# Optimization experiments

Hardware: AMD Instinct MI355X
Metric: run time of the kernel (lower is better)

Reference implementation:

```python
import jax, jax.numpy as jnp
import numpy as np


def blockdiag_matmul(x, w):
    """Block-diagonal (Monarch) linear: w has shape (nblocks, out_blk, in_blk);
    x has shape (..., nblocks*in_blk); returns (..., nblocks*out_blk)."""
    nb, q, p = w.shape
    lead = x.shape[:-1]
    xb = x.reshape(-1, nb, p)  # (tokens, nblocks, in_blk)
    out = jnp.einsum('bnp,nqp->bnq', xb, w)  # per-block matmul
    return out.reshape(*lead, nb * q)


def setup_inputs() -> dict:
    key = jax.random.key(0)
    k_x, k1, k2, k3 = jax.random.split(key, 4)
    B, S, D = 4, 4096, 2048
    NB, FF = 4, 8192  # nblocks, adjusted intermediate size
    # Kaiming-uniform-like scale for block weights (fan_in = D or FF per block-row)
    s1 = 1.0 / np.sqrt(D)
    s2 = 1.0 / np.sqrt(FF)
    return {
        'x': jax.random.normal(k_x, (B, S, D), dtype=jnp.float32),
        'w1': jax.random.normal(k1, (NB, FF // NB, D // NB), dtype=jnp.float32) * s1,
        'w3': jax.random.normal(k3, (NB, FF // NB, D // NB), dtype=jnp.float32) * s1,
        'w2': jax.random.normal(k2, (NB, D // NB, FF // NB), dtype=jnp.float32) * s2,
    }


def reference(x, w1, w3, w2):
    # SwiGLU MLP: w2(silu(w1(x)) * w3(x)), all projections block-diagonal
    gate = jax.nn.silu(blockdiag_matmul(x, w1))
    up = blockdiag_matmul(x, w3)
    return blockdiag_matmul(gate * up, w2)
```

## Files before the change

### kernel.cpp

```cpp
#include <hip/hip_runtime.h>
#include <cstdint>

typedef __attribute__((ext_vector_type(8))) short bf16x8;
typedef __attribute__((ext_vector_type(4))) float f32x4;
typedef unsigned short u16;

#define RD(p) (*(const bf16x8*)(p))

__device__ inline u16 f2bf(float f) {
  union { float f; unsigned int u; } v; v.f = f;
  unsigned int u = v.u;
  unsigned int r = (u + 0x7fffu + ((u >> 16) & 1u)) >> 16;
  return (u16)r;
}

__device__ inline void gload_lds16(const u16* g, u16* l) {
  __builtin_amdgcn_global_load_lds(
      (const __attribute__((address_space(1))) void*)g,
      (__attribute__((address_space(3))) void*)l, 16, 0, 0);
}

#define PH_BEGIN() \
  __builtin_amdgcn_s_barrier(); \
  asm volatile("s_waitcnt lgkmcnt(0)" ::: "memory"); \
  __builtin_amdgcn_s_setprio(1)
#define PH_END() \
  __builtin_amdgcn_s_setprio(0); \
  __builtin_amdgcn_s_barrier()

__global__ void cvt_f32_bf16(const float* __restrict__ src, u16* __restrict__ dst, int n8) {
  int i = blockIdx.x * blockDim.x + threadIdx.x;
  int stride = gridDim.x * blockDim.x;
  for (; i < n8; i += stride) {
    const float4* s = (const float4*)(src + (size_t)i * 8);
    float4 a = s[0], b = s[1];
    union { u16 h[8]; uint4 v; } o;
    o.h[0] = f2bf(a.x); o.h[1] = f2bf(a.y); o.h[2] = f2bf(a.z); o.h[3] = f2bf(a.w);
    o.h[4] = f2bf(b.x); o.h[5] = f2bf(b.y); o.h[6] = f2bf(b.z); o.h[7] = f2bf(b.w);
    *(uint4*)(dst + (size_t)i * 8) = o.v;
  }
}

__global__ void cvt_w3x(const float* __restrict__ s0, const float* __restrict__ s1,
                        const float* __restrict__ s2, u16* __restrict__ d0,
                        u16* __restrict__ d1, u16* __restrict__ d2) {
  const int n8 = 524288;
  int i = blockIdx.x * blockDim.x + threadIdx.x;
  int stride = gridDim.x * blockDim.x;
  for (; i < 3 * n8; i += stride) {
    int seg = i / n8;
    int j = i - seg * n8;
    const float* src = (seg == 0) ? s0 : (seg == 1) ? s1 : s2;
    u16* dst = (seg == 0) ? d0 : (seg == 1) ? d1 : d2;
    const float4* s = (const float4*)(src + (size_t)j * 8);
    float4 a = s[0], b = s[1];
    union { u16 h[8]; uint4 v; } o;
    o.h[0] = f2bf(a.x); o.h[1] = f2bf(a.y); o.h[2] = f2bf(a.z); o.h[3] = f2bf(a.w);
    o.h[4] = f2bf(b.x); o.h[5] = f2bf(b.y); o.h[6] = f2bf(b.z); o.h[7] = f2bf(b.w);
    *(uint4*)(dst + (size_t)j * 8) = o.v;
  }
}

__launch_bounds__(512, 2)
__global__ void gemm_gateup8(const u16* __restrict__ xb, const u16* __restrict__ w1b,
                             const u16* __restrict__ w3b, u16* __restrict__ hout) {
  constexpr int NT = 8;
  constexpr int TPB = 4;
  constexpr int TOT = NT * TPB;
  __shared__ __attribute__((aligned(16))) u16 lA[2][256 * 64];
  __shared__ __attribute__((aligned(16))) u16 lB[2][2][128 * 64];

  int bid = blockIdx.x;
  int sw = (bid & 7) * 128 + (bid >> 3);
  int nblk = sw >> 8;
  int rem = sw & 255;
  int mt = rem >> 2, ntg = rem & 3;

  int tid = threadIdx.x, w = tid >> 6, ln = tid & 63;
  int wr = w >> 1, wc = w & 1;
  int l15 = ln & 15, l4 = ln >> 4;
  int lr = ln >> 3, ln8 = ln & 7;

  int cx0 = ((l4 ^ (l15 & 7)) << 4);
  int cx1 = (((4 + l4) ^ (l15 & 7)) << 4);
  int aOff0 = (wr * 64 + l15) * 128 + cx0;
  int aOff1 = (wr * 64 + l15) * 128 + cx1;
  int bOff0 = (wc * 64 + l15) * 128 + cx0;
  int bOff1 = (wc * 64 + l15) * 128 + cx1;

  int u0t = w * 8, u1t = 64 + w * 8;
  int rbA0 = ((u0t >> 5) << 6) + (u0t & 31);
  int rbA1 = ((u1t >> 5) << 6) + (u1t & 31);
  int dA0 = rbA0 * 128, dA1 = rbA1 * 128;
  int dB0 = u0t * 128, dB1 = u1t * 128;
  int gaA0 = rbA0 * 2048, gaA1 = rbA1 * 2048;
  int gaB0 = u0t * 512, gaB1 = u1t * 512;
  int swzg = (ln8 ^ lr) << 3;

  const u16* gA  = xb  + (size_t)(mt * 256) * 2048 + nblk * 512 + lr * 2048 + swzg;
  const u16* gB1 = w1b + (size_t)nblk * (2048 * 512) + (size_t)(ntg * 512) * 512 + lr * 512 + swzg;
  const u16* gB3 = w3b + (size_t)nblk * (2048 * 512) + (size_t)(ntg * 512) * 512 + lr * 512 + swzg;

  #define OFFA(s) (((s) & 7) * 64)
  #define OFFB(s) ((((s) >> 3) << 16) + (((s) & 7) * 64))

  f32x4 acc1[4][4], acc3[4][4];
#pragma unroll
  for (int i = 0; i < 4; i++)
#pragma unroll
    for (int j = 0; j < 4; j++) {
      acc1[i][j] = (f32x4){0.f, 0.f, 0.f, 0.f};
      acc3[i][j] = (f32x4){0.f, 0.f, 0.f, 0.f};
    }

  gload_lds16(gA + gaA0,              (u16*)((char*)lA + dA0));
  gload_lds16(gA + gaA1,              (u16*)((char*)lA + dA1));
  gload_lds16(gB3 + gaB0,             (u16*)((char*)lB + 16384 + dB0));
  gload_lds16(gB3 + gaB1,             (u16*)((char*)lB + 16384 + dB1));
  gload_lds16(gA + gaA0 + 65536,      (u16*)((char*)lA + dA0 + 4096));
  gload_lds16(gA + gaA1 + 65536,      (u16*)((char*)lA + dA1 + 4096));
  gload_lds16(gB1 + gaB0,             (u16*)((char*)lB + dB0));
  gload_lds16(gB1 + gaB1,             (u16*)((char*)lB + dB1));
  gload_lds16(gA + OFFA(1) + gaA0,          (u16*)((char*)lA + 32768 + dA0));
  gload_lds16(gA + OFFA(1) + gaA1,          (u16*)((char*)lA + 32768 + dA1));
  gload_lds16(gB3 + OFFB(1) + gaB0,         (u16*)((char*)lB + 32768 + 16384 + dB0));
  gload_lds16(gB3 + OFFB(1) + gaB1,         (u16*)((char*)lB + 32768 + 16384 + dB1));
  gload_lds16(gA + OFFA(1) + gaA0 + 65536,  (u16*)((char*)lA + 32768 + dA0 + 4096));
  gload_lds16(gA + OFFA(1) + gaA1 + 65536,  (u16*)((char*)lA + 32768 + dA1 + 4096));
  asm volatile("s_waitcnt vmcnt(6)" ::: "memory");
  __builtin_amdgcn_s_barrier();

  int sCur = 0, sNxt = 32768;
  bf16x8 aT[2][2], aH[2][2], b1[4][2], b3[4][2];

  for (int kt = 0; kt < TOT; ++kt) {
    const char* pA0 = (const char*)lA + (sCur + aOff0);
    const char* pA1 = (const char*)lA + (sCur + aOff1);
    const char* pB0 = (const char*)lB + (sCur + bOff0);
    const char* pB1p = (const char*)lB + (sCur + bOff1);
    int s1 = kt + 1, s2 = kt + 2;
    int oA2 = OFFA(s2), oB1n = OFFB(s1), oB32 = OFFB(s2);
    bool q1 = (s1 < TOT), q2 = (s2 < TOT);

#pragma unroll
    for (int f = 0; f < 2; ++f) {
      aT[f][0] = RD(pA0 + f * 2048); aT[f][1] = RD(pA1 + f * 2048);
    }
#pragma unroll
    for (int g = 0; g < 4; ++g) {
      b1[g][0] = RD(pB0 + g * 2048); b1[g][1] = RD(pB1p + g * 2048);
    }
    if (q1) {
      gload_lds16(gB1 + oB1n + gaB0, (u16*)((char*)lB + sNxt + dB0));
      gload_lds16(gB1 + oB1n + gaB1, (u16*)((char*)lB + sNxt + dB1));
    }
    asm volatile("s_waitcnt lgkmcnt(8)" ::: "memory");
    PH_BEGIN();
#pragma unroll
    for (int f = 0; f < 2; ++f)
#pragma unroll
      for (int g = 0; g < 4; ++g)
#pragma unroll
        for (int ks = 0; ks < 2; ++ks)
          acc1[f][g] = __builtin_amdgcn_mfma_f32_16x16x32_bf16(b1[g][ks], aT[f][ks], acc1[f][g], 0, 0, 0);
    PH_END();

#pragma unroll
    for (int g = 0; g < 4; ++g) {
      b3[g][0] = RD(pB0 + 16384 + g * 2048); b3[g][1] = RD(pB1p + 16384 + g * 2048);
    }
    if (q2) {
      gload_lds16(gA + oA2 + gaA0, (u16*)((char*)lA + sCur + dA0));
      gload_lds16(gA + oA2 + gaA1, (u16*)((char*)lA + sCur + dA1));
    }
    PH_BEGIN();
#pragma unroll
    for (int f = 0; f < 2; ++f)
#pragma unroll
      for (int g = 0; g < 4; ++g)
#pragma unroll
        for (int ks = 0; ks < 2; ++ks)
          acc3[f][g] = __builtin_amdgcn_mfma_f32_16x16x32_bf16(b3[g][ks], aT[f][ks], acc3[f][g], 0, 0, 0);
    PH_END();

#pragma unroll
    for (int f = 0; f < 2; ++f) {
      aH[f][0] = RD(pA0 + 4096 + f * 2048); aH[f][1] = RD(pA1 + 4096 + f * 2048);
    }
    if (q2) {
      gload_lds16(gB3 + oB32 + gaB0, (u16*)((char*)lB + sCur + 16384 + dB0));
      gload_lds16(gB3 + oB32 + gaB1, (u16*)((char*)lB + sCur + 16384 + dB1));
    }
    PH_BEGIN();
#pragma unroll
    for (int f = 0; f < 2; ++f)
#pragma unroll
      for (int g = 0; g < 4; ++g)
#pragma unroll
        for (int ks = 0; ks < 2; ++ks)
          acc1[2 + f][g] = __builtin_amdgcn_mfma_f32_16x16x32_bf16(b1[g][ks], aH[f][ks], acc1[2 + f][g], 0, 0, 0);
    PH_END();

    if (q2) {
      gload_lds16(gA + oA2 + gaA0 + 65536, (u16*)((char*)lA + sCur + dA0 + 4096));
      gload_lds16(gA + oA2 + gaA1 + 65536, (u16*)((char*)lA + sCur + dA1 + 4096));
    }
    PH_BEGIN();
#pragma unroll
    for (int f = 0; f < 2; ++f)
#pragma unroll
      for (int g = 0; g < 4; ++g)
#pragma unroll
        for (int ks = 0; ks < 2; ++ks)
          acc3[2 + f][g] = __builtin_amdgcn_mfma_f32_16x16x32_bf16(b3[g][ks], aH[f][ks], acc3[2 + f][g], 0, 0, 0);
    __builtin_amdgcn_s_setprio(0);
    if (kt < TOT - 2)       asm volatile("s_waitcnt vmcnt(6)" ::: "memory");
    else if (kt == TOT - 2) asm volatile("s_waitcnt vmcnt(0)" ::: "memory");
    __builtin_amdgcn_s_barrier();
    sCur ^= 32768; sNxt ^= 32768;

    if ((kt & 7) == 7) {
      int nt = ntg * 4 + (kt >> 3);
      u16* Hb = hout + (size_t)(mt * 256 + wr * 64) * 8192 + nblk * 2048 + nt * 128 + wc * 64;
#pragma unroll
      for (int f = 0; f < 4; ++f) {
        u16* Hrow = Hb + (size_t)(f * 16 + l15) * 8192 + l4 * 4;
#pragma unroll
        for (int g = 0; g < 4; ++g) {
          union { u16 h[4]; uint2 v; } o;
#pragma unroll
          for (int r = 0; r < 4; ++r) {
            float gate = acc1[f][g][r];
            float up = acc3[f][g][r];
            float s = gate * __builtin_amdgcn_rcpf(1.f + __expf(-gate));
            o.h[r] = f2bf(s * up);
          }
          *(uint2*)(Hrow + g * 16) = o.v;
        }
      }
#pragma unroll
      for (int i = 0; i < 4; i++)
#pragma unroll
        for (int j = 0; j < 4; j++) {
          acc1[i][j] = (f32x4){0.f, 0.f, 0.f, 0.f};
          acc3[i][j] = (f32x4){0.f, 0.f, 0.f, 0.f};
        }
    }
  }
  #undef OFFA
  #undef OFFB
}

__launch_bounds__(512, 2)
__global__ void gemm_down8(const u16* __restrict__ hmat, const u16* __restrict__ w2b,
                           float* __restrict__ out) {
  constexpr int NT = 32;
  __shared__ __attribute__((aligned(16))) u16 lA[2][256 * 64];
  __shared__ __attribute__((aligned(16))) u16 lB[2][256 * 64];

  int bid = blockIdx.x;
  int sw = (bid & 7) * 64 + (bid >> 3);
  int nblk = sw >> 7;
  int rem = sw & 127;
  int mt = rem >> 1, nt = rem & 1;

  int tid = threadIdx.x, w = tid >> 6, ln = tid & 63;
  int mi = w >> 2, nj = w & 3;
  int l15 = ln & 15, l4 = ln >> 4;
  int lr = ln >> 3, ln8 = ln & 7;

  int cx0 = ((l4 ^ (l15 & 7)) << 4);
  int cx1 = (((4 + l4) ^ (l15 & 7)) << 4);
  int aOff0 = (mi * 128 + l15) * 128 + cx0;
  int aOff1 = (mi * 128 + l15) * 128 + cx1;
  int bOff0 = (nj * 64 + l15) * 128 + cx0;
  int bOff1 = (nj * 64 + l15) * 128 + cx1;

  int u0t = w * 8, u1t = 64 + w * 8;
  int dA0 = u0t * 128, dA1 = (64 + u1t) * 128;
  int rbB0 = ((u0t >> 5) << 6) + (u0t & 31);
  int rbB1 = ((u1t >> 5) << 6) + (u1t & 31);
  int dB0 = rbB0 * 128, dB1 = rbB1 * 128;
  int gaA0 = u0t * 8192, gaA1 = (64 + u1t) * 8192;
  int gaB0 = rbB0 * 2048, gaB1 = rbB1 * 2048;
  int swzg = (ln8 ^ lr) << 3;

  const u16* gA = hmat + (size_t)(mt * 256) * 8192 + nblk * 2048 + lr * 8192 + swzg;
  const u16* gB = w2b + (size_t)nblk * (512 * 2048) + (size_t)(nt * 256) * 2048 + lr * 2048 + swzg;

  f32x4 acc[8][4];
#pragma unroll
  for (int i = 0; i < 8; i++)
#pragma unroll
    for (int j = 0; j < 4; j++) acc[i][j] = (f32x4){0.f, 0.f, 0.f, 0.f};

  gload_lds16(gA + gaA0,           (u16*)((char*)lA + dA0));
  gload_lds16(gA + gaA1,           (u16*)((char*)lA + dA1));
  gload_lds16(gB + gaB0 + 65536,   (u16*)((char*)lB + dB0 + 4096));
  gload_lds16(gB + gaB1 + 65536,   (u16*)((char*)lB + dB1 + 4096));
  gload_lds16(gA + gaA0 + 524288,  (u16*)((char*)lA + dA0 + 8192));
  gload_lds16(gA + gaA1 + 524288,  (u16*)((char*)lA + dA1 + 8192));
  gload_lds16(gB + gaB0,           (u16*)((char*)lB + dB0));
  gload_lds16(gB + gaB1,           (u16*)((char*)lB + dB1));
  gload_lds16(gA + 64 + gaA0,          (u16*)((char*)lA + 32768 + dA0));
  gload_lds16(gA + 64 + gaA1,          (u16*)((char*)lA + 32768 + dA1));
  gload_lds16(gB + 64 + gaB0 + 65536,  (u16*)((char*)lB + 32768 + dB0 + 4096));
  gload_lds16(gB + 64 + gaB1 + 65536,  (u16*)((char*)lB + 32768 + dB1 + 4096));
  gload_lds16(gA + 64 + gaA0 + 524288, (u16*)((char*)lA + 32768 + dA0 + 8192));
  gload_lds16(gA + 64 + gaA1 + 524288, (u16*)((char*)lA + 32768 + dA1 + 8192));
  gA += 128; gB += 64;
  asm volatile("s_waitcnt vmcnt(6)" ::: "memory");
  __builtin_amdgcn_s_barrier();

  int sCur = 0, sNxt = 32768;
  bf16x8 aF[4][2], bLo[2][2], bHi[2][2];

  for (int kt = 0; kt < NT; ++kt) {
    const char* pA0 = (const char*)lA + (sCur + aOff0);
    const char* pA1 = (const char*)lA + (sCur + aOff1);
    const char* pB0 = (const char*)lB + (sCur + bOff0);
    const char* pB1p = (const char*)lB + (sCur + bOff1);
    bool s1 = (kt + 1 < NT), s2 = (kt + 2 < NT);

#pragma unroll
    for (int f = 0; f < 4; ++f) {
      aF[f][0] = RD(pA0 + f * 2048); aF[f][1] = RD(pA1 + f * 2048);
    }
#pragma unroll
    for (int g = 0; g < 2; ++g) {
      bLo[g][0] = RD(pB0 + g * 2048); bLo[g][1] = RD(pB1p + g * 2048);
    }
    if (s1) {
      gload_lds16(gB + gaB0, (u16*)((char*)lB + sNxt + dB0));
      gload_lds16(gB + gaB1, (u16*)((char*)lB + sNxt + dB1));
    }
    asm volatile("s_waitcnt lgkmcnt(8)" ::: "memory");
    PH_BEGIN();
#pragma unroll
    for (int f = 0; f < 4; ++f)
#pragma unroll
      for (int g = 0; g < 2; ++g)
#pragma unroll
        for (int ks = 0; ks < 2; ++ks)
          acc[f][g] = __builtin_amdgcn_mfma_f32_16x16x32_bf16(bLo[g][ks], aF[f][ks], acc[f][g], 0, 0, 0);
    PH_END();

#pragma unroll
    for (int g = 0; g < 2; ++g) {
      bHi[g][0] = RD(pB0 + 4096 + g * 2048); bHi[g][1] = RD(pB1p + 4096 + g * 2048);
    }
    if (s2) {
      gload_lds16(gA + gaA0, (u16*)((char*)lA + sCur + dA0));
      gload_lds16(gA + gaA1, (u16*)((char*)lA + sCur + dA1));
    }
    PH_BEGIN();
#pragma unroll
    for (int f = 0; f < 4; ++f)
#pragma unroll
      for (int g = 0; g < 2; ++g)
#pragma unroll
        for (int ks = 0; ks < 2; ++ks)
          acc[f][2 + g] = __builtin_amdgcn_mfma_f32_16x16x32_bf16(bHi[g][ks], aF[f][ks], acc[f][2 + g], 0, 0, 0);
    PH_END();

#pragma unroll
    for (int f = 0; f < 4; ++f) {
      aF[f][0] = RD(pA0 + 8192 + f * 2048); aF[f][1] = RD(pA1 + 8192 + f * 2048);
    }
    if (s2) {
      gload_lds16(gB + 64 + gaB0 + 65536, (u16*)((char*)lB + sCur + dB0 + 4096));
      gload_lds16(gB + 64 + gaB1 + 65536, (u16*)((char*)lB + sCur + dB1 + 4096));
    }
    PH_BEGIN();
#pragma unroll
    for (int f = 0; f < 4; ++f)
#pragma unroll
      for (int g = 0; g < 2; ++g)
#pragma unroll
        for (int ks = 0; ks < 2; ++ks)
          acc[4 + f][g] = __builtin_amdgcn_mfma_f32_16x16x32_bf16(bLo[g][ks], aF[f][ks], acc[4 + f][g], 0, 0, 0);
    PH_END();

    if (s2) {
      gload_lds16(gA + gaA0 + 524288, (u16*)((char*)lA + sCur + dA0 + 8192));
      gload_lds16(gA + gaA1 + 524288, (u16*)((char*)lA + sCur + dA1 + 8192));
    }
    PH_BEGIN();
#pragma unroll
    for (int f = 0; f < 4; ++f)
#pragma unroll
      for (int g = 0; g < 2; ++g)
#pragma unroll
        for (int ks = 0; ks < 2; ++ks)
          acc[4 + f][2 + g] = __builtin_amdgcn_mfma_f32_16x16x32_bf16(bHi[g][ks], aF[f][ks], acc[4 + f][2 + g], 0, 0, 0);
    __builtin_amdgcn_s_setprio(0);
    if (kt < NT - 2)       asm volatile("s_waitcnt vmcnt(6)" ::: "memory");
    else if (kt == NT - 2) asm volatile("s_waitcnt vmcnt(0)" ::: "memory");
    __builtin_amdgcn_s_barrier();
    gA += 64; gB += 64;
    sCur ^= 32768; sNxt ^= 32768;
  }

  float* Ob = out + (size_t)(mt * 256 + mi * 128) * 2048 + nblk * 512 + nt * 256 + nj * 64;
#pragma unroll
  for (int f = 0; f < 8; ++f) {
    float* Orow = Ob + (size_t)(f * 16 + l15) * 2048 + l4 * 4;
#pragma unroll
    for (int g = 0; g < 4; ++g)
      *(f32x4*)(Orow + g * 16) = acc[f][g];
  }
}

extern "C" void kernel_launch(void* const* d_in, const int* in_sizes, int n_in,
                              void* d_out, int out_size, void* d_ws, size_t ws_size,
                              hipStream_t stream) {
  const float* x  = (const float*)d_in[0];
  const float* w1 = (const float*)d_in[1];
  const float* w3 = (const float*)d_in[2];
  const float* w2 = (const float*)d_in[3];

  char* ws = (char*)d_ws;
  u16* xb  = (u16*)(ws);
  u16* w1b = (u16*)(ws + 67108864);
  u16* w3b = (u16*)(ws + 75497472);
  u16* w2b = (u16*)(ws + 83886080);
  u16* h   = (u16*)(ws + 92274688);

  cvt_w3x<<<2048, 256, 0, stream>>>(w1, w3, w2, w1b, w3b, w2b);
  cvt_f32_bf16<<<2048, 256, 0, stream>>>(x, xb, 33554432 / 8);

  gemm_gateup8<<<1024, 512, 0, stream>>>(xb, w1b, w3b, h);
  gemm_down8<<<512, 512, 0, stream>>>(h, w2b, (float*)d_out);
}
```

Measured before the change: 569.0 us.

## Restructure GEMM main loops from four to two barrier phases per k-step

Both GEMM kernels merge their four MFMA phases per k-iteration into two larger phases, each issuing more MFMAs. Global-to-LDS prefetch loads are regrouped into two batches per iteration and the vmcnt waits are adjusted to match. The aim is to halve the barrier and phase-switching overhead per k-step. In exchange, LDS fragment reads are batched up front, which raises register pressure and reduces the interleaving of loads with compute.

New measurement: 484.8 us, median of 2. 1.17x faster.

```diff
diff --git a/kernel.cpp b/kernel.cpp
--- a/kernel.cpp
+++ b/kernel.cpp
@@ -62,7 +62,7 @@
 }
 
 __launch_bounds__(512, 2)
-__global__ void gemm_gateup8(const u16* __restrict__ xb, const u16* __restrict__ w1b,
+__global__ void gemm_gateup2(const u16* __restrict__ xb, const u16* __restrict__ w1b,
                              const u16* __restrict__ w3b, u16* __restrict__ hout) {
   constexpr int NT = 8;
   constexpr int TPB = 4;
@@ -113,25 +113,23 @@
       acc3[i][j] = (f32x4){0.f, 0.f, 0.f, 0.f};
     }
 
-  gload_lds16(gA + gaA0,              (u16*)((char*)lA + dA0));
-  gload_lds16(gA + gaA1,              (u16*)((char*)lA + dA1));
-  gload_lds16(gB3 + gaB0,             (u16*)((char*)lB + 16384 + dB0));
-  gload_lds16(gB3 + gaB1,             (u16*)((char*)lB + 16384 + dB1));
-  gload_lds16(gA + gaA0 + 65536,      (u16*)((char*)lA + dA0 + 4096));
-  gload_lds16(gA + gaA1 + 65536,      (u16*)((char*)lA + dA1 + 4096));
-  gload_lds16(gB1 + gaB0,             (u16*)((char*)lB + dB0));
-  gload_lds16(gB1 + gaB1,             (u16*)((char*)lB + dB1));
-  gload_lds16(gA + OFFA(1) + gaA0,          (u16*)((char*)lA + 32768 + dA0));
-  gload_lds16(gA + OFFA(1) + gaA1,          (u16*)((char*)lA + 32768 + dA1));
-  gload_lds16(gB3 + OFFB(1) + gaB0,         (u16*)((char*)lB + 32768 + 16384 + dB0));
-  gload_lds16(gB3 + OFFB(1) + gaB1,         (u16*)((char*)lB + 32768 + 16384 + dB1));
-  gload_lds16(gA + OFFA(1) + gaA0 + 65536,  (u16*)((char*)lA + 32768 + dA0 + 4096));
-  gload_lds16(gA + OFFA(1) + gaA1 + 65536,  (u16*)((char*)lA + 32768 + dA1 + 4096));
-  asm volatile("s_waitcnt vmcnt(6)" ::: "memory");
+  gload_lds16(gA + gaA0,          (u16*)((char*)lA + dA0));
+  gload_lds16(gA + gaA1,          (u16*)((char*)lA + dA1));
+  gload_lds16(gA + gaA0 + 65536,  (u16*)((char*)lA + dA0 + 4096));
+  gload_lds16(gA + gaA1 + 65536,  (u16*)((char*)lA + dA1 + 4096));
+  gload_lds16(gB1 + gaB0,         (u16*)((char*)lB + dB0));
+  gload_lds16(gB1 + gaB1,         (u16*)((char*)lB + dB1));
+  gload_lds16(gB3 + gaB0,         (u16*)((char*)lB + 16384 + dB0));
+  gload_lds16(gB3 + gaB1,         (u16*)((char*)lB + 16384 + dB1));
+  gload_lds16(gA + OFFA(1) + gaA0,         (u16*)((char*)lA + 32768 + dA0));
+  gload_lds16(gA + OFFA(1) + gaA1,         (u16*)((char*)lA + 32768 + dA1));
+  gload_lds16(gA + OFFA(1) + gaA0 + 65536, (u16*)((char*)lA + 32768 + dA0 + 4096));
+  gload_lds16(gA + OFFA(1) + gaA1 + 65536, (u16*)((char*)lA + 32768 + dA1 + 4096));
+  asm volatile("s_waitcnt vmcnt(4)" ::: "memory");
   __builtin_amdgcn_s_barrier();
 
   int sCur = 0, sNxt = 32768;
-  bf16x8 aT[2][2], aH[2][2], b1[4][2], b3[4][2];
+  bf16x8 aT[4][2], bb[4][2];
 
   for (int kt = 0; kt < TOT; ++kt) {
     const char* pA0 = (const char*)lA + (sCur + aOff0);
@@ -139,82 +137,54 @@
     const char* pB0 = (const char*)lB + (sCur + bOff0);
     const char* pB1p = (const char*)lB + (sCur + bOff1);
     int s1 = kt + 1, s2 = kt + 2;
-    int oA2 = OFFA(s2), oB1n = OFFB(s1), oB32 = OFFB(s2);
+    int oA2 = OFFA(s2), oBn = OFFB(s1);
     bool q1 = (s1 < TOT), q2 = (s2 < TOT);
 
 #pragma unroll
     for (int f = 0; f < 2; ++f) {
-      aT[f][0] = RD(pA0 + f * 2048); aT[f][1] = RD(pA1 + f * 2048);
+      aT[f][0] = RD(pA0 + f * 2048);        aT[f][1] = RD(pA1 + f * 2048);
+      aT[2 + f][0] = RD(pA0 + 4096 + f * 2048); aT[2 + f][1] = RD(pA1 + 4096 + f * 2048);
     }
 #pragma unroll
     for (int g = 0; g < 4; ++g) {
-      b1[g][0] = RD(pB0 + g * 2048); b1[g][1] = RD(pB1p + g * 2048);
+      bb[g][0] = RD(pB0 + g * 2048); bb[g][1] = RD(pB1p + g * 2048);
     }
     if (q1) {
-      gload_lds16(gB1 + oB1n + gaB0, (u16*)((char*)lB + sNxt + dB0));
-      gload_lds16(gB1 + oB1n + gaB1, (u16*)((char*)lB + sNxt + dB1));
-    }
-    asm volatile("s_waitcnt lgkmcnt(8)" ::: "memory");
+      gload_lds16(gB1 + oBn + gaB0, (u16*)((char*)lB + sNxt + dB0));
+      gload_lds16(gB1 + oBn + gaB1, (u16*)((char*)lB + sNxt + dB1));
+      gload_lds16(gB3 + oBn + gaB0, (u16*)((char*)lB + sNxt + 16384 + dB0));
+      gload_lds16(gB3 + oBn + gaB1, (u16*)((char*)lB + sNxt + 16384 + dB1));
+    }
     PH_BEGIN();
 #pragma unroll
-    for (int f = 0; f < 2; ++f)
+    for (int f = 0; f < 4; ++f)
 #pragma unroll
       for (int g = 0; g < 4; ++g)
 #pragma unroll
         for (int ks = 0; ks < 2; ++ks)
-          acc1[f][g] = __builtin_amdgcn_mfma_f32_16x16x32_bf16(b1[g][ks], aT[f][ks], acc1[f][g], 0, 0, 0);
+          acc1[f][g] = __builtin_amdgcn_mfma_f32_16x16x32_bf16(bb[g][ks], aT[f][ks], acc1[f][g], 0, 0, 0);
     PH_END();
 
 #pragma unroll
     for (int g = 0; g < 4; ++g) {
-      b3[g][0] = RD(pB0 + 16384 + g * 2048); b3[g][1] = RD(pB1p + 16384 + g * 2048);
+      bb[g][0] = RD(pB0 + 16384 + g * 2048); bb[g][1] = RD(pB1p + 16384 + g * 2048);
     }
     if (q2) {
-      gload_lds16(gA + oA2 + gaA0, (u16*)((char*)lA + sCur + dA0));
-      gload_lds16(gA + oA2 + gaA1, (u16*)((char*)lA + sCur + dA1));
-    }
-    PH_BEGIN();
-#pragma unroll
-    for (int f = 0; f < 2; ++f)
-#pragma unroll
-      for (int g = 0; g < 4; ++g)
-#pragma unroll
-        for (int ks = 0; ks < 2; ++ks)
-          acc3[f][g] = __builtin_amdgcn_mfma_f32_16x16x32_bf16(b3[g][ks], aT[f][ks], acc3[f][g], 0, 0, 0);
-    PH_END();
-
-#pragma unroll
-    for (int f = 0; f < 2; ++f) {
-      aH[f][0] = RD(pA0 + 4096 + f * 2048); aH[f][1] = RD(pA1 + 4096 + f * 2048);
-    }
-    if (q2) {
-      gload_lds16(gB3 + oB32 + gaB0, (u16*)((char*)lB + sCur + 16384 + dB0));
-      gload_lds16(gB3 + oB32 + gaB1, (u16*)((char*)lB + sCur + 16384 + dB1));
-    }
-    PH_BEGIN();
-#pragma unroll
-    for (int f = 0; f < 2; ++f)
-#pragma unroll
-      for (int g = 0; g < 4; ++g)
-#pragma unroll
-        for (int ks = 0; ks < 2; ++ks)
-          acc1[2 + f][g] = __builtin_amdgcn_mfma_f32_16x16x32_bf16(b1[g][ks], aH[f][ks], acc1[2 + f][g], 0, 0, 0);
-    PH_END();
-
-    if (q2) {
+      gload_lds16(gA + oA2 + gaA0,         (u16*)((char*)lA + sCur + dA0));
+      gload_lds16(gA + oA2 + gaA1,         (u16*)((char*)lA + sCur + dA1));
       gload_lds16(gA + oA2 + gaA0 + 65536, (u16*)((char*)lA + sCur + dA0 + 4096));
       gload_lds16(gA + oA2 + gaA1 + 65536, (u16*)((char*)lA + sCur + dA1 + 4096));
     }
     PH_BEGIN();
 #pragma unroll
-    for (int f = 0; f < 2; ++f)
+    for (int f = 0; f < 4; ++f)
 #pragma unroll
       for (int g = 0; g < 4; ++g)
 #pragma unroll
         for (int ks = 0; ks < 2; ++ks)
-          acc3[2 + f][g] = __builtin_amdgcn_mfma_f32_16x16x32_bf16(b3[g][ks], aH[f][ks], acc3[2 + f][g], 0, 0, 0);
+          acc3[f][g] = __builtin_amdgcn_mfma_f32_16x16x32_bf16(bb[g][ks], aT[f][ks], acc3[f][g], 0, 0, 0);
     __builtin_amdgcn_s_setprio(0);
-    if (kt < TOT - 2)       asm volatile("s_waitcnt vmcnt(6)" ::: "memory");
+    if (kt < TOT - 2)       asm volatile("s_waitcnt vmcnt(4)" ::: "memory");
     else if (kt == TOT - 2) asm volatile("s_waitcnt vmcnt(0)" ::: "memory");
     __builtin_amdgcn_s_barrier();
     sCur ^= 32768; sNxt ^= 32768;
@@ -252,7 +222,7 @@
 }
 
 __launch_bounds__(512, 2)
-__global__ void gemm_down8(const u16* __restrict__ hmat, const u16* __restrict__ w2b,
+__global__ void gemm_down2(const u16* __restrict__ hmat, const u16* __restrict__ w2b,
                            float* __restrict__ out) {
   constexpr int NT = 32;
   __shared__ __attribute__((aligned(16))) u16 lA[2][256 * 64];
@@ -294,22 +264,19 @@
 #pragma unroll
     for (int j = 0; j < 4; j++) acc[i][j] = (f32x4){0.f, 0.f, 0.f, 0.f};
 
-  gload_lds16(gA + gaA0,           (u16*)((char*)lA + dA0));
-  gload_lds16(gA + gaA1,           (u16*)((char*)lA + dA1));
-  gload_lds16(gB + gaB0 + 65536,   (u16*)((char*)lB + dB0 + 4096));
-  gload_lds16(gB + gaB1 + 65536,   (u16*)((char*)lB + dB1 + 4096));
-  gload_lds16(gA + gaA0 + 524288,  (u16*)((char*)lA + dA0 + 8192));
-  gload_lds16(gA + gaA1 + 524288,  (u16*)((char*)lA + dA1 + 8192));
-  gload_lds16(gB + gaB0,           (u16*)((char*)lB + dB0));
-  gload_lds16(gB + gaB1,           (u16*)((char*)lB + dB1));
-  gload_lds16(gA + 64 + gaA0,          (u16*)((char*)lA + 32768 + dA0));
-  gload_lds16(gA + 64 + gaA1,          (u16*)((char*)lA + 32768 + dA1));
-  gload_lds16(gB + 64 + gaB0 + 65536,  (u16*)((char*)lB + 32768 + dB0 + 4096));
-  gload_lds16(gB + 64 + gaB1 + 65536,  (u16*)((char*)lB + 32768 + dB1 + 4096));
-  gload_lds16(gA + 64 + gaA0 + 524288, (u16*)((char*)lA + 32768 + dA0 + 8192));
-  gload_lds16(gA + 64 + gaA1 + 524288, (u16*)((char*)lA + 32768 + dA1 + 8192));
-  gA += 128; gB += 64;
-  asm volatile("s_waitcnt vmcnt(6)" ::: "memory");
+  gload_lds16(gA + gaA0,            (u16*)((char*)lA + dA0));
+  gload_lds16(gA + gaA1,            (u16*)((char*)lA + dA1));
+  gload_lds16(gA + gaA0 + 524288,   (u16*)((char*)lA + dA0 + 8192));
+  gload_lds16(gA + gaA1 + 524288,   (u16*)((char*)lA + dA1 + 8192));
+  gload_lds16(gB + gaB0,            (u16*)((char*)lB + dB0));
+  gload_lds16(gB + gaB1,            (u16*)((char*)lB + dB1));
+  gload_lds16(gB + gaB0 + 65536,    (u16*)((char*)lB + dB0 + 4096));
+  gload_lds16(gB + gaB1 + 65536,    (u16*)((char*)lB + dB1 + 4096));
+  gload_lds16(gA + 64 + gaA0,           (u16*)((char*)lA + 32768 + dA0));
+  gload_lds16(gA + 64 + gaA1,           (u16*)((char*)lA + 32768 + dA1));
+  gload_lds16(gB + 64 + gaB0 + 65536,   (u16*)((char*)lB + 32768 + dB0 + 4096));
+  gload_lds16(gB + 64 + gaB1 + 65536,   (u16*)((char*)lB + 32768 + dB1 + 4096));
+  asm volatile("s_waitcnt vmcnt(4)" ::: "memory");
   __builtin_amdgcn_s_barrier();
 
   int sCur = 0, sNxt = 32768;
@@ -320,7 +287,8 @@
     const char* pA1 = (const char*)lA + (sCur + aOff1);
     const char* pB0 = (const char*)lB + (sCur + bOff0);
     const char* pB1p = (const char*)lB + (sCur + bOff1);
-    bool s1 = (kt + 1 < NT), s2 = (kt + 2 < NT);
+    int kO1 = (kt + 1) * 64, kO2 = (kt + 2) * 64;
+    bool q1 = (kt + 1 < NT), q2 = (kt + 2 < NT);
 
 #pragma unroll
     for (int f = 0; f < 4; ++f) {
@@ -328,48 +296,36 @@
     }
 #pragma unroll
     for (int g = 0; g < 2; ++g) {
-      bLo[g][0] = RD(pB0 + g * 2048); bLo[g][1] = RD(pB1p + g * 2048);
-    }
-    if (s1) {
-      gload_lds16(gB + gaB0, (u16*)((char*)lB + sNxt + dB0));
-      gload_lds16(gB + gaB1, (u16*)((char*)lB + sNxt + dB1));
-    }
-    asm volatile("s_waitcnt lgkmcnt(8)" ::: "memory");
+      bLo[g][0] = RD(pB0 + g * 2048);        bLo[g][1] = RD(pB1p + g * 2048);
+      bHi[g][0] = RD(pB0 + 4096 + g * 2048); bHi[g][1] = RD(pB1p + 4096 + g * 2048);
+    }
+    if (q1) {
+      gload_lds16(gB + kO1 + gaB0,          (u16*)((char*)lB + sNxt + dB0));
+      gload_lds16(gB + kO1 + gaB1,          (u16*)((char*)lB + sNxt + dB1));
+      gload_lds16(gA + kO1 + gaA0 + 524288, (u16*)((char*)lA + sNxt + dA0 + 8192));
+      gload_lds16(gA + kO1 + gaA1 + 524288, (u16*)((char*)lA + sNxt + dA1 + 8192));
+    }
     PH_BEGIN();
 #pragma unroll
     for (int f = 0; f < 4; ++f)
 #pragma unroll
       for (int g = 0; g < 2; ++g)
 #pragma unroll
-        for (int ks = 0; ks < 2; ++ks)
-          acc[f][g] = __builtin_amdgcn_mfma_f32_16x16x32_bf16(bLo[g][ks], aF[f][ks], acc[f][g], 0, 0, 0);
-    PH_END();
-
-#pragma unroll
-    for (int g = 0; g < 2; ++g) {
-      bHi[g][0] = RD(pB0 + 4096 + g * 2048); bHi[g][1] = RD(pB1p + 4096 + g * 2048);
-    }
-    if (s2) {
-      gload_lds16(gA + gaA0, (u16*)((char*)lA + sCur + dA0));
-      gload_lds16(gA + gaA1, (u16*)((char*)lA + sCur + dA1));
-    }
-    PH_BEGIN();
-#pragma unroll
-    for (int f = 0; f < 4; ++f)
-#pragma unroll
-      for (int g = 0; g < 2; ++g)
-#pragma unroll
-        for (int ks = 0; ks < 2; ++ks)
+        for (int ks = 0; ks < 2; ++ks) {
+          acc[f][g]     = __builtin_amdgcn_mfma_f32_16x16x32_bf16(bLo[g][ks], aF[f][ks], acc[f][g], 0, 0, 0);
           acc[f][2 + g] = __builtin_amdgcn_mfma_f32_16x16x32_bf16(bHi[g][ks], aF[f][ks], acc[f][2 + g], 0, 0, 0);
+        }
     PH_END();
 
 #pragma unroll
     for (int f = 0; f < 4; ++f) {
       aF[f][0] = RD(pA0 + 8192 + f * 2048); aF[f][1] = RD(pA1 + 8192 + f * 2048);
     }
-    if (s2) {
-      gload_lds16(gB + 64 + gaB0 + 65536, (u16*)((char*)lB + sCur + dB0 + 4096));
-      gload_lds16(gB + 64 + gaB1 + 65536, (u16*)((char*)lB + sCur + dB1 + 4096));
+    if (q2) {
+      gload_lds16(gA + kO2 + gaA0,         (u16*)((char*)lA + sCur + dA0));
+      gload_lds16(gA + kO2 + gaA1,         (u16*)((char*)lA + sCur + dA1));
+      gload_lds16(gB + kO2 + gaB0 + 65536, (u16*)((char*)lB + sCur + dB0 + 4096));
+      gload_lds16(gB + kO2 + gaB1 + 65536, (u16*)((char*)lB + sCur + dB1 + 4096));
     }
     PH_BEGIN();
 #pragma unroll
@@ -377,27 +333,14 @@
 #pragma unroll
       for (int g = 0; g < 2; ++g)
 #pragma unroll
-        for (int ks = 0; ks < 2; ++ks)
-          acc[4 + f][g] = __builtin_amdgcn_mfma_f32_16x16x32_bf16(bLo[g][ks], aF[f][ks], acc[4 + f][g], 0, 0, 0);
-    PH_END();
-
-    if (s2) {
-      gload_lds16(gA + gaA0 + 524288, (u16*)((char*)lA + sCur + dA0 + 8192));
-      gload_lds16(gA + gaA1 + 524288, (u16*)((char*)lA + sCur + dA1 + 8192));
-    }
-    PH_BEGIN();
-#pragma unroll
-    for (int f = 0; f < 4; ++f)
-#pragma unroll
-      for (int g = 0; g < 2; ++g)
-#pragma unroll
-        for (int ks = 0; ks < 2; ++ks)
+        for (int ks = 0; ks < 2; ++ks) {
+          acc[4 + f][g]     = __builtin_amdgcn_mfma_f32_16x16x32_bf16(bLo[g][ks], aF[f][ks], acc[4 + f][g], 0, 0, 0);
           acc[4 + f][2 + g] = __builtin_amdgcn_mfma_f32_16x16x32_bf16(bHi[g][ks], aF[f][ks], acc[4 + f][2 + g], 0, 0, 0);
+        }
     __builtin_amdgcn_s_setprio(0);
-    if (kt < NT - 2)       asm volatile("s_waitcnt vmcnt(6)" ::: "memory");
+    if (kt < NT - 2)       asm volatile("s_waitcnt vmcnt(4)" ::: "memory");
     else if (kt == NT - 2) asm volatile("s_waitcnt vmcnt(0)" ::: "memory");
     __builtin_amdgcn_s_barrier();
-    gA += 64; gB += 64;
     sCur ^= 32768; sNxt ^= 32768;
   }
 
@@ -429,6 +372,6 @@
   cvt_w3x<<<2048, 256, 0, stream>>>(w1, w3, w2, w1b, w3b, w2b);
   cvt_f32_bf16<<<2048, 256, 0, stream>>>(x, xb, 33554432 / 8);
 
-  gemm_gateup8<<<1024, 512, 0, stream>>>(xb, w1b, w3b, h);
-  gemm_down8<<<512, 512, 0, stream>>>(h, w2b, (float*)d_out);
-}
+  gemm_gateup2<<<1024, 512, 0, stream>>>(xb, w1b, w3b, h);
+  gemm_down2<<<512, 512, 0, stream>>>(h, w2b, (float*)d_out);
+}
```
